# Kernel optimization log

Hardware: AMD Instinct MI355X
Metric: run time of the kernel (lower is better)

The kernel has to match this reference:

```python
import jax, jax.numpy as jnp
import numpy as np

BUCKET_SIZE = 128
HEADS = 8
HEAD_DIM = 64
LOOK_BACKWARD = 1
LOOK_FORWARD = 0  # causal => no look forward
TOKEN_SELF_ATTN_VALUE = -50000.0


def look_around(x, backward, forward, pad_value):
    n = x.shape[1]
    pw = [(0, 0)] * x.ndim
    pw[1] = (backward, forward)
    px = jnp.pad(x, pw, constant_values=pad_value)
    return jnp.concatenate([px[:, i:i + n] for i in range(backward + forward + 1)], axis=2)


def shift(x):
    # relative-shift trick: (..., i, j) -> (..., i, j)
    *lead, i, j = x.shape
    x = jnp.concatenate([x, jnp.zeros((*lead, i, i), x.dtype)], axis=-1)
    l = i + j - 1
    x = x.reshape(*lead, i * (i + j))
    pad = (-x.shape[-1]) % l
    x = jnp.concatenate([x, jnp.zeros((*lead, pad), x.dtype)], axis=-1)
    x = x.reshape(*lead, -1, l)
    return x[..., :i, i - 1:]


def setup_inputs() -> dict:
    key = jax.random.key(0)
    kq, kk, kv, kr = jax.random.split(key, 4)
    B, H, T, E = 2, HEADS, 8192, HEAD_DIM
    q = jax.random.normal(kq, (B, H, T, E), dtype=jnp.float32)
    k = jax.random.normal(kk, (B, H, T, E), dtype=jnp.float32)
    v = jax.random.normal(kv, (B, H, T, E), dtype=jnp.float32)
    rel_weights = jax.random.normal(kr, (2 * BUCKET_SIZE, H, E), dtype=jnp.float32)
    return {"q": q, "k": k, "v": v, "rel_weights": rel_weights}


def reference(q, k, v, rel_weights):
    B, H, T, E = q.shape
    qm = q.reshape(B * H, T, E)
    km = k.reshape(B * H, T, E)
    vm = v.reshape(B * H, T, E)

    # shared_qk: l2-normalize keys (F.normalize with eps=1e-12)
    km = km / jnp.maximum(jnp.linalg.norm(km, axis=-1, keepdims=True), 1e-12)

    buckets = T // BUCKET_SIZE
    bq = qm.reshape(B * H, buckets, BUCKET_SIZE, E)
    bk = km.reshape(B * H, buckets, BUCKET_SIZE, E)
    bv = vm.reshape(B * H, buckets, BUCKET_SIZE, E)

    bk = look_around(bk, LOOK_BACKWARD, LOOK_FORWARD, -1.0)
    bv = look_around(bv, LOOK_BACKWARD, LOOK_FORWARD, -1.0)

    ticker = jnp.arange(T, dtype=q.dtype)
    bq_t = ticker.reshape(1, buckets, BUCKET_SIZE)
    bq_k = look_around(bq_t, LOOK_BACKWARD, LOOK_FORWARD, -1.0)

    scale = E ** -0.5
    dots = jnp.einsum('bnie,bnje->bnij', bq, bk) * scale

    # relative positional bias
    bq5 = bq.reshape(B, H, buckets, BUCKET_SIZE, E)
    emb = jnp.einsum('bhnid,jhd->bhnij', bq5, rel_weights) * scale
    dots = dots + shift(emb).reshape(dots.shape)

    mask_value = -jnp.finfo(dots.dtype).max
    # shared_qk: mask self-attention positions
    self_mask = bq_t[:, :, :, None] == bq_k[:, :, None, :]
    dots = jnp.where(self_mask, TOKEN_SELF_ATTN_VALUE, dots)
    # causal mask
    causal_mask = bq_t[:, :, :, None] < bq_k[:, :, None, :]
    dots = jnp.where(causal_mask, mask_value, dots)
    # look-around padding mask
    pad_mask = (bq_k == -1.0)[:, :, None, :]
    dots = jnp.where(pad_mask, mask_value, dots)

    attn = jax.nn.softmax(dots, axis=-1)
    out = jnp.einsum('bnij,bnje->bnie', attn, bv)
    return out.reshape(B, H, T, E)
```

## Files before the change

### kernel.cpp

```cpp
#include <hip/hip_runtime.h>
#include <hip/hip_bf16.h>
#include <float.h>

#define NHEAD 8

typedef __attribute__((ext_vector_type(8))) short bf16x8;
typedef __attribute__((ext_vector_type(4))) float f32x4;

static __device__ __forceinline__ unsigned short bfb(float f) {
    __hip_bfloat16 h = __float2bfloat16(f);
    unsigned short u; __builtin_memcpy(&u, &h, 2); return u;
}
static __device__ __forceinline__ unsigned int pk2(float a, float b) {
    return (unsigned int)bfb(a) | ((unsigned int)bfb(b) << 16);
}
static __device__ __forceinline__ float bf2f_lo(unsigned int u) { return __uint_as_float(u << 16); }
static __device__ __forceinline__ float bf2f_hi(unsigned int u) { return __uint_as_float(u & 0xffff0000u); }

static __device__ __forceinline__ int swz64(int r, int c) {
    return (r << 6) + (c ^ ((r & 7) << 3));
}
static __device__ __forceinline__ int vIdx(int c, int kk) {
    return (c << 8) + (kk ^ ((c & 31) << 3));
}
static __device__ __forceinline__ int pIdx(int wv, int row, int col) {
    const int ch = (col >> 3) ^ (row & 3);
    return (wv * 16 + row) * 40 + ch * 8 + (col & 7);
}

static __device__ __forceinline__ f32x4 mfma16(bf16x8 a, bf16x8 b, f32x4 c) {
    return __builtin_amdgcn_mfma_f32_16x16x32_bf16(a, b, c, 0, 0, 0);
}

__global__ __launch_bounds__(512, 4)
void local_attn_kernel(const float* __restrict__ qg, const float* __restrict__ kg,
                       const float* __restrict__ vg, const float* __restrict__ rwg,
                       float* __restrict__ outg)
{
    __shared__ __align__(16) unsigned short sB[256 * 64];
    __shared__ __align__(16) unsigned short sRW[256 * 64];
    __shared__ __align__(16) unsigned short sP[8 * 16 * 40];

    const int tid  = threadIdx.x;
    const int lane = tid & 63;
    const int wv   = tid >> 6;
    const int jl   = lane & 15;
    const int hi   = lane >> 4;

    const int lb = ((blockIdx.x & 7) << 7) + (blockIdx.x >> 3);
    const int bh = lb >> 6;
    const int n  = lb & 63;
    const int h  = bh & 7;

    const float scale = 0.125f;
    const size_t bhOff = (size_t)bh * 8192 * 64;

    const float* Qp = qg + bhOff + (size_t)n * 128 * 64;
    const float* Kp = kg + bhOff + ((long)n - 1) * 128 * 64;
    const float* Vp = vg + bhOff + ((long)n - 1) * 128 * 64;

    const int cr = tid >> 4;
    const int c0 = (tid & 15) << 2;

    const int vc  = tid & 63;
    const int vkb = (tid >> 6) << 5;
    const bool vzero = (n == 0 && vkb < 128);
    unsigned int vpk[16];
    #pragma unroll
    for (int u = 0; u < 16; ++u) {
        float a = 0.f, b = 0.f;
        if (!vzero) {
            a = Vp[(vkb + 2 * u) * 64 + vc];
            b = Vp[(vkb + 2 * u + 1) * 64 + vc];
        }
        vpk[u] = pk2(a, b);
    }
    #pragma unroll
    for (int u = 0; u < 16; ++u)
        asm volatile("" :: "v"(vpk[u]));

    #pragma unroll
    for (int pp = 0; pp < 8; ++pp) {
        const int row = pp * 32 + cr;
        f32x4 x = {0.f, 0.f, 0.f, 0.f};
        if (!(n == 0 && row < 128))
            x = *reinterpret_cast<const f32x4*>(Kp + row * 64 + c0);
        float ss = x[0] * x[0] + x[1] * x[1] + x[2] * x[2] + x[3] * x[3];
        ss += __shfl_xor(ss, 1);
        ss += __shfl_xor(ss, 2);
        ss += __shfl_xor(ss, 4);
        ss += __shfl_xor(ss, 8);
        const float rn = 1.0f / fmaxf(sqrtf(ss), 1e-12f);
        ushort4 pkk = make_ushort4(bfb(x[0] * rn), bfb(x[1] * rn),
                                   bfb(x[2] * rn), bfb(x[3] * rn));
        *reinterpret_cast<ushort4*>(&sB[swz64(row, c0)]) = pkk;
    }

    #pragma unroll
    for (int pp = 0; pp < 8; ++pp) {
        const int row = pp * 32 + cr;
        const f32x4 x = *reinterpret_cast<const f32x4*>(rwg + ((size_t)row * NHEAD + h) * 64 + c0);
        ushort4 pkw = make_ushort4(bfb(x[0]), bfb(x[1]), bfb(x[2]), bfb(x[3]));
        *reinterpret_cast<ushort4*>(&sRW[swz64(row, c0)]) = pkw;
    }

    const int arow = wv * 16 + jl;
    const int kq0  = hi << 3;
    const float* qr = Qp + arow * 64 + kq0;
    const f32x4 qa = *reinterpret_cast<const f32x4*>(qr);
    const f32x4 qb = *reinterpret_cast<const f32x4*>(qr + 4);
    const f32x4 qc = *reinterpret_cast<const f32x4*>(qr + 32);
    const f32x4 qd = *reinterpret_cast<const f32x4*>(qr + 36);
    bf16x8 aq0, aq1;
    #pragma unroll
    for (int q = 0; q < 4; ++q) {
        aq0[q]     = (short)bfb(qa[q] * scale);
        aq0[q + 4] = (short)bfb(qb[q] * scale);
        aq1[q]     = (short)bfb(qc[q] * scale);
        aq1[q + 4] = (short)bfb(qd[q] * scale);
    }

    __syncthreads();

    const int tMax = wv + 8;

    f32x4 dots[16] = {};
    __builtin_amdgcn_s_setprio(1);
    #pragma unroll
    for (int t = 0; t < 16; ++t) {
        if (t <= tMax) {
            const int rr = t * 16 + jl;
            const bf16x8 b0 = *reinterpret_cast<const bf16x8*>(&sB[swz64(rr, kq0)]);
            const bf16x8 b1 = *reinterpret_cast<const bf16x8*>(&sB[swz64(rr, 32 + kq0)]);
            f32x4 d = {0.f, 0.f, 0.f, 0.f};
            d = mfma16(aq0, b0, d);
            d = mfma16(aq1, b1, d);
            dots[t] = d;
        }
    }
    __builtin_amdgcn_s_setprio(0);

    const int cv0 = 4 * hi + 1, cv1 = 4 * hi + 2, cv2 = 4 * hi + 3, cv3 = 4 * hi + 4;
    const int sl0 = (hi << 4) | ((jl - cv0) & 15);
    const int sl1 = (hi << 4) | ((jl - cv1) & 15);
    const int sl2 = (hi << 4) | ((jl - cv2) & 15);
    const int sl3 = (hi << 4) | ((jl - cv3) & 15);
    const bool g0 = jl >= cv0, g1 = jl >= cv1, g2 = jl >= cv2, g3 = jl >= cv3;

    unsigned int cur01, cur23;
    {
        const int rr = (7 - wv) * 16 + jl;
        const bf16x8 b0 = *reinterpret_cast<const bf16x8*>(&sRW[swz64(rr, kq0)]);
        const bf16x8 b1 = *reinterpret_cast<const bf16x8*>(&sRW[swz64(rr, 32 + kq0)]);
        f32x4 e = {0.f, 0.f, 0.f, 0.f};
        e = mfma16(aq0, b0, e);
        e = mfma16(aq1, b1, e);
        cur01 = pk2(e[0], e[1]);
        cur23 = pk2(e[2], e[3]);
    }
    unsigned int lo0 = (unsigned int)__shfl((int)cur01, sl0);
    unsigned int lo1 = (unsigned int)__shfl((int)cur01, sl1);
    unsigned int lo2 = (unsigned int)__shfl((int)cur23, sl2);
    unsigned int lo3 = (unsigned int)__shfl((int)cur23, sl3);

    unsigned int p01[16] = {}, p23[16] = {};
    float sm[4] = {0.f, 0.f, 0.f, 0.f};
    const bool npad = (n == 0);

    #pragma unroll
    for (int t = 0; t < 16; ++t) {
        if (t <= tMax) {
            unsigned int n01 = 0, n23 = 0;
            const int ts = t + 8 - wv;
            if (ts < 16) {
                const int rr2 = ts * 16 + jl;
                const bf16x8 e0 = *reinterpret_cast<const bf16x8*>(&sRW[swz64(rr2, kq0)]);
                const bf16x8 e1 = *reinterpret_cast<const bf16x8*>(&sRW[swz64(rr2, 32 + kq0)]);
                f32x4 e = {0.f, 0.f, 0.f, 0.f};
                e = mfma16(aq0, e0, e);
                e = mfma16(aq1, e1, e);
                n01 = pk2(e[0], e[1]);
                n23 = pk2(e[2], e[3]);
            }
            const unsigned int h0 = (unsigned int)__shfl((int)n01, sl0);
            const unsigned int h1 = (unsigned int)__shfl((int)n01, sl1);
            const unsigned int h2 = (unsigned int)__shfl((int)n23, sl2);
            const unsigned int h3 = (unsigned int)__shfl((int)n23, sl3);
            f32x4 d = dots[t];
            d[0] += bf2f_lo(g0 ? h0 : lo0);
            d[1] += bf2f_hi(g1 ? h1 : lo1);
            d[2] += bf2f_lo(g2 ? h2 : lo2);
            d[3] += bf2f_hi(g3 ? h3 : lo3);
            lo0 = h0; lo1 = h1; lo2 = h2; lo3 = h3;
            if (t >= 8 && t == tMax) {
                #pragma unroll
                for (int r = 0; r < 4; ++r) {
                    const int dd = 128 + jl - 4 * hi - r;
                    float x = d[r];
                    x = (dd == 128) ? -50.0f : x;
                    x = (dd > 128) ? -3.0e38f : x;
                    d[r] = x;
                }
            }
            if (t < 8 && npad) {
                #pragma unroll
                for (int r = 0; r < 4; ++r) d[r] = -3.0e38f;
            }
            f32x4 pe;
            #pragma unroll
            for (int r = 0; r < 4; ++r) {
                pe[r] = __expf(d[r]);
                sm[r] += pe[r];
            }
            p01[t] = pk2(pe[0], pe[1]);
            p23[t] = pk2(pe[2], pe[3]);
        }
    }

    float rinv[4];
    #pragma unroll
    for (int r = 0; r < 4; ++r) {
        sm[r] += __shfl_xor(sm[r], 1);
        sm[r] += __shfl_xor(sm[r], 2);
        sm[r] += __shfl_xor(sm[r], 4);
        sm[r] += __shfl_xor(sm[r], 8);
        rinv[r] = 1.0f / sm[r];
    }

    __syncthreads();

    #pragma unroll
    for (int w4 = 0; w4 < 4; ++w4) {
        const uint4 w = make_uint4(vpk[4 * w4], vpk[4 * w4 + 1],
                                   vpk[4 * w4 + 2], vpk[4 * w4 + 3]);
        *reinterpret_cast<uint4*>(&sB[vIdx(vc, vkb + 8 * w4)]) = w;
    }

    __syncthreads();

    f32x4 o[4] = {};
    #pragma unroll
    for (int pv = 0; pv < 8; ++pv) {
        if (2 * pv <= tMax) {
            #pragma unroll
            for (int tt = 0; tt < 2; ++tt) {
                const int t = 2 * pv + tt;
                const unsigned int w01 = p01[t];
                const unsigned int w23 = p23[t];
                const int col = tt * 16 + jl;
                sP[pIdx(wv, 4 * hi + 0, col)] = (unsigned short)w01;
                sP[pIdx(wv, 4 * hi + 1, col)] = (unsigned short)(w01 >> 16);
                sP[pIdx(wv, 4 * hi + 2, col)] = (unsigned short)w23;
                sP[pIdx(wv, 4 * hi + 3, col)] = (unsigned short)(w23 >> 16);
            }
            const bf16x8 pa = *reinterpret_cast<const bf16x8*>(&sP[pIdx(wv, jl, kq0)]);
            __builtin_amdgcn_s_setprio(1);
            #pragma unroll
            for (int ct = 0; ct < 4; ++ct) {
                const bf16x8 vb = *reinterpret_cast<const bf16x8*>(&sB[vIdx(ct * 16 + jl, pv * 32 + kq0)]);
                o[ct] = mfma16(pa, vb, o[ct]);
            }
            __builtin_amdgcn_s_setprio(0);
        }
    }

    const int ibase = wv * 16 + (hi << 2);
    float* Op = outg + bhOff + (size_t)n * 128 * 64;
    #pragma unroll
    for (int ct = 0; ct < 4; ++ct)
        #pragma unroll
        for (int r = 0; r < 4; ++r)
            Op[(ibase + r) * 64 + ct * 16 + jl] = o[ct][r] * rinv[r];
}

extern "C" void kernel_launch(void* const* d_in, const int* in_sizes, int n_in,
                              void* d_out, int out_size, void* d_ws, size_t ws_size,
                              hipStream_t stream) {
    const float* q  = (const float*)d_in[0];
    const float* k  = (const float*)d_in[1];
    const float* v  = (const float*)d_in[2];
    const float* rw = (const float*)d_in[3];
    float* out = (float*)d_out;
    local_attn_kernel<<<dim3(1024), dim3(512), 0, stream>>>(q, k, v, rw, out);
}
```

Before: 58.77 us.

## Process two buckets per 1024-thread block to share K/V/rel-weight loads

Each block now handles two adjacent query buckets with 16 waves, loading a 384-row K/V window and the relative-weight table once for both, so the overlapping neighbour bucket and the rel weights are no longer loaded and converted twice. V goes into its own LDS buffer with a new swizzle, which removes the extra barriers and the register staging of V. Softmax probabilities stay in the fp32 dots registers and are packed to bf16 only just before the PV step. The cost is a larger LDS footprint (about 128 KB) and launch bounds of 1024 threads with one block, which lowers occupancy and raises register pressure per wave.

```diff
diff --git a/kernel.cpp b/kernel.cpp
--- a/kernel.cpp
+++ b/kernel.cpp
@@ -21,7 +21,9 @@
     return (r << 6) + (c ^ ((r & 7) << 3));
 }
 static __device__ __forceinline__ int vIdx(int c, int kk) {
-    return (c << 8) + (kk ^ ((c & 31) << 3));
+    const int blk = kk >> 7, k7 = kk & 127;
+    const int ch  = ((k7 >> 3) ^ (c & 15));
+    return c * 384 + blk * 128 + ch * 8 + (kk & 7);
 }
 static __device__ __forceinline__ int pIdx(int wv, int row, int col) {
     const int ch = (col >> 3) ^ (row & 3);
@@ -32,59 +34,64 @@
     return __builtin_amdgcn_mfma_f32_16x16x32_bf16(a, b, c, 0, 0, 0);
 }
 
-__global__ __launch_bounds__(512, 4)
+__global__ __launch_bounds__(1024, 1)
 void local_attn_kernel(const float* __restrict__ qg, const float* __restrict__ kg,
                        const float* __restrict__ vg, const float* __restrict__ rwg,
                        float* __restrict__ outg)
 {
-    __shared__ __align__(16) unsigned short sB[256 * 64];
+    __shared__ __align__(16) unsigned short sK[384 * 64];
+    __shared__ __align__(16) unsigned short sV[64 * 384];
     __shared__ __align__(16) unsigned short sRW[256 * 64];
-    __shared__ __align__(16) unsigned short sP[8 * 16 * 40];
+    __shared__ __align__(16) unsigned short sP[16 * 16 * 40];
 
     const int tid  = threadIdx.x;
     const int lane = tid & 63;
     const int wv   = tid >> 6;
+    const int wvL  = wv & 7;
+    const int bkt  = wv >> 3;
     const int jl   = lane & 15;
     const int hi   = lane >> 4;
 
-    const int lb = ((blockIdx.x & 7) << 7) + (blockIdx.x >> 3);
-    const int bh = lb >> 6;
-    const int n  = lb & 63;
+    const int lb = ((blockIdx.x & 7) << 6) + (blockIdx.x >> 3);
+    const int bh = lb >> 5;
+    const int nb = (lb & 31) << 1;
     const int h  = bh & 7;
 
     const float scale = 0.125f;
     const size_t bhOff = (size_t)bh * 8192 * 64;
-
-    const float* Qp = qg + bhOff + (size_t)n * 128 * 64;
-    const float* Kp = kg + bhOff + ((long)n - 1) * 128 * 64;
-    const float* Vp = vg + bhOff + ((long)n - 1) * 128 * 64;
-
-    const int cr = tid >> 4;
-    const int c0 = (tid & 15) << 2;
-
-    const int vc  = tid & 63;
-    const int vkb = (tid >> 6) << 5;
-    const bool vzero = (n == 0 && vkb < 128);
-    unsigned int vpk[16];
-    #pragma unroll
-    for (int u = 0; u < 16; ++u) {
-        float a = 0.f, b = 0.f;
-        if (!vzero) {
-            a = Vp[(vkb + 2 * u) * 64 + vc];
-            b = Vp[(vkb + 2 * u + 1) * 64 + vc];
-        }
-        vpk[u] = pk2(a, b);
-    }
-    #pragma unroll
-    for (int u = 0; u < 16; ++u)
-        asm volatile("" :: "v"(vpk[u]));
-
-    #pragma unroll
-    for (int pp = 0; pp < 8; ++pp) {
-        const int row = pp * 32 + cr;
+    const int n = nb + bkt;
+
+    const float* Kw = kg + bhOff + ((long)nb - 1) * 128 * 64;
+    const float* Vw = vg + bhOff + ((long)nb - 1) * 128 * 64;
+
+    const int cr6 = tid >> 4;
+    const int c0  = (tid & 15) << 2;
+
+    {
+        const int vc = tid & 63;
+        const int vg0 = (tid >> 6) * 24;
+        unsigned int vp[12];
+        #pragma unroll
+        for (int u = 0; u < 12; ++u) {
+            const int k0 = vg0 + 2 * u;
+            float a = 0.f, b = 0.f;
+            if (!(nb == 0 && k0 < 128))       a = Vw[(size_t)k0 * 64 + vc];
+            if (!(nb == 0 && (k0 + 1) < 128)) b = Vw[(size_t)(k0 + 1) * 64 + vc];
+            vp[u] = pk2(a, b);
+        }
+        #pragma unroll
+        for (int w4 = 0; w4 < 3; ++w4) {
+            const uint4 w = make_uint4(vp[4 * w4], vp[4 * w4 + 1], vp[4 * w4 + 2], vp[4 * w4 + 3]);
+            *reinterpret_cast<uint4*>(&sV[vIdx(vc, vg0 + 8 * w4)]) = w;
+        }
+    }
+
+    #pragma unroll
+    for (int pp = 0; pp < 6; ++pp) {
+        const int row = pp * 64 + cr6;
         f32x4 x = {0.f, 0.f, 0.f, 0.f};
-        if (!(n == 0 && row < 128))
-            x = *reinterpret_cast<const f32x4*>(Kp + row * 64 + c0);
+        if (!(nb == 0 && row < 128))
+            x = *reinterpret_cast<const f32x4*>(Kw + (size_t)row * 64 + c0);
         float ss = x[0] * x[0] + x[1] * x[1] + x[2] * x[2] + x[3] * x[3];
         ss += __shfl_xor(ss, 1);
         ss += __shfl_xor(ss, 2);
@@ -93,20 +100,20 @@
         const float rn = 1.0f / fmaxf(sqrtf(ss), 1e-12f);
         ushort4 pkk = make_ushort4(bfb(x[0] * rn), bfb(x[1] * rn),
                                    bfb(x[2] * rn), bfb(x[3] * rn));
-        *reinterpret_cast<ushort4*>(&sB[swz64(row, c0)]) = pkk;
-    }
-
-    #pragma unroll
-    for (int pp = 0; pp < 8; ++pp) {
-        const int row = pp * 32 + cr;
+        *reinterpret_cast<ushort4*>(&sK[swz64(row, c0)]) = pkk;
+    }
+
+    #pragma unroll
+    for (int pp = 0; pp < 4; ++pp) {
+        const int row = pp * 64 + cr6;
         const f32x4 x = *reinterpret_cast<const f32x4*>(rwg + ((size_t)row * NHEAD + h) * 64 + c0);
         ushort4 pkw = make_ushort4(bfb(x[0]), bfb(x[1]), bfb(x[2]), bfb(x[3]));
         *reinterpret_cast<ushort4*>(&sRW[swz64(row, c0)]) = pkw;
     }
 
-    const int arow = wv * 16 + jl;
+    const int arow = wvL * 16 + jl;
     const int kq0  = hi << 3;
-    const float* qr = Qp + arow * 64 + kq0;
+    const float* qr = qg + bhOff + (size_t)n * 128 * 64 + arow * 64 + kq0;
     const f32x4 qa = *reinterpret_cast<const f32x4*>(qr);
     const f32x4 qb = *reinterpret_cast<const f32x4*>(qr + 4);
     const f32x4 qc = *reinterpret_cast<const f32x4*>(qr + 32);
@@ -122,16 +129,17 @@
 
     __syncthreads();
 
-    const int tMax = wv + 8;
+    const int tMax = wvL + 8;
+    const int bOff = bkt << 7;
 
     f32x4 dots[16] = {};
     __builtin_amdgcn_s_setprio(1);
     #pragma unroll
     for (int t = 0; t < 16; ++t) {
         if (t <= tMax) {
-            const int rr = t * 16 + jl;
-            const bf16x8 b0 = *reinterpret_cast<const bf16x8*>(&sB[swz64(rr, kq0)]);
-            const bf16x8 b1 = *reinterpret_cast<const bf16x8*>(&sB[swz64(rr, 32 + kq0)]);
+            const int rr = bOff + t * 16 + jl;
+            const bf16x8 b0 = *reinterpret_cast<const bf16x8*>(&sK[swz64(rr, kq0)]);
+            const bf16x8 b1 = *reinterpret_cast<const bf16x8*>(&sK[swz64(rr, 32 + kq0)]);
             f32x4 d = {0.f, 0.f, 0.f, 0.f};
             d = mfma16(aq0, b0, d);
             d = mfma16(aq1, b1, d);
@@ -149,7 +157,7 @@
 
     unsigned int cur01, cur23;
     {
-        const int rr = (7 - wv) * 16 + jl;
+        const int rr = (7 - wvL) * 16 + jl;
         const bf16x8 b0 = *reinterpret_cast<const bf16x8*>(&sRW[swz64(rr, kq0)]);
         const bf16x8 b1 = *reinterpret_cast<const bf16x8*>(&sRW[swz64(rr, 32 + kq0)]);
         f32x4 e = {0.f, 0.f, 0.f, 0.f};
@@ -163,7 +171,6 @@
     unsigned int lo2 = (unsigned int)__shfl((int)cur23, sl2);
     unsigned int lo3 = (unsigned int)__shfl((int)cur23, sl3);
 
-    unsigned int p01[16] = {}, p23[16] = {};
     float sm[4] = {0.f, 0.f, 0.f, 0.f};
     const bool npad = (n == 0);
 
@@ -171,7 +178,7 @@
     for (int t = 0; t < 16; ++t) {
         if (t <= tMax) {
             unsigned int n01 = 0, n23 = 0;
-            const int ts = t + 8 - wv;
+            const int ts = t + 8 - wvL;
             if (ts < 16) {
                 const int rr2 = ts * 16 + jl;
                 const bf16x8 e0 = *reinterpret_cast<const bf16x8*>(&sRW[swz64(rr2, kq0)]);
@@ -206,14 +213,13 @@
                 #pragma unroll
                 for (int r = 0; r < 4; ++r) d[r] = -3.0e38f;
             }
-            f32x4 pe;
             #pragma unroll
             for (int r = 0; r < 4; ++r) {
-                pe[r] = __expf(d[r]);
-                sm[r] += pe[r];
-            }
-            p01[t] = pk2(pe[0], pe[1]);
-            p23[t] = pk2(pe[2], pe[3]);
+                const float pe = __expf(d[r]);
+                d[r] = pe;
+                sm[r] += pe;
+            }
+            dots[t] = d;
         }
     }
 
@@ -227,17 +233,6 @@
         rinv[r] = 1.0f / sm[r];
     }
 
-    __syncthreads();
-
-    #pragma unroll
-    for (int w4 = 0; w4 < 4; ++w4) {
-        const uint4 w = make_uint4(vpk[4 * w4], vpk[4 * w4 + 1],
-                                   vpk[4 * w4 + 2], vpk[4 * w4 + 3]);
-        *reinterpret_cast<uint4*>(&sB[vIdx(vc, vkb + 8 * w4)]) = w;
-    }
-
-    __syncthreads();
-
     f32x4 o[4] = {};
     #pragma unroll
     for (int pv = 0; pv < 8; ++pv) {
@@ -245,8 +240,11 @@
             #pragma unroll
             for (int tt = 0; tt < 2; ++tt) {
                 const int t = 2 * pv + tt;
-                const unsigned int w01 = p01[t];
-                const unsigned int w23 = p23[t];
+                unsigned int w01 = 0, w23 = 0;
+                if (t <= tMax) {
+                    w01 = pk2(dots[t][0], dots[t][1]);
+                    w23 = pk2(dots[t][2], dots[t][3]);
+                }
                 const int col = tt * 16 + jl;
                 sP[pIdx(wv, 4 * hi + 0, col)] = (unsigned short)w01;
                 sP[pIdx(wv, 4 * hi + 1, col)] = (unsigned short)(w01 >> 16);
@@ -257,14 +255,14 @@
             __builtin_amdgcn_s_setprio(1);
             #pragma unroll
             for (int ct = 0; ct < 4; ++ct) {
-                const bf16x8 vb = *reinterpret_cast<const bf16x8*>(&sB[vIdx(ct * 16 + jl, pv * 32 + kq0)]);
+                const bf16x8 vb = *reinterpret_cast<const bf16x8*>(&sV[vIdx(ct * 16 + jl, bOff + pv * 32 + kq0)]);
                 o[ct] = mfma16(pa, vb, o[ct]);
             }
             __builtin_amdgcn_s_setprio(0);
         }
     }
 
-    const int ibase = wv * 16 + (hi << 2);
+    const int ibase = wvL * 16 + (hi << 2);
     float* Op = outg + bhOff + (size_t)n * 128 * 64;
     #pragma unroll
     for (int ct = 0; ct < 4; ++ct)
@@ -281,5 +279,5 @@
     const float* v  = (const float*)d_in[2];
     const float* rw = (const float*)d_in[3];
     float* out = (float*)d_out;
-    local_attn_kernel<<<dim3(1024), dim3(512), 0, stream>>>(q, k, v, rw, out);
-}
+    local_attn_kernel<<<dim3(512), dim3(1024), 0, stream>>>(q, k, v, rw, out);
+}
```

Result: no change. 58.88 us (+0.2%).

## Fuse QK scores and softmax into PV loop, stage V directly to LDS

Applied to the files above, without the earlier changes.

V is now written straight into a dedicated LDS buffer instead of being held in 16 packed registers until after softmax. The relative-position products are computed first from a bf16 copy of the weights staged in the shared buffer, then normalized K replaces them in the same buffer. The QK^T MFMAs, bias add, masking and exp are then computed per tile inside the PV loop, so the full dots/probability register arrays are gone and the final row-sum reduction moves to the end. This is meant to cut register pressure and interleave softmax with PV MFMAs, at the cost of two extra barriers and keeping K in registers across the relative-position phase.

```diff
diff --git a/kernel.cpp b/kernel.cpp
--- a/kernel.cpp
+++ b/kernel.cpp
@@ -38,7 +38,7 @@
                        float* __restrict__ outg)
 {
     __shared__ __align__(16) unsigned short sB[256 * 64];
-    __shared__ __align__(16) unsigned short sRW[256 * 64];
+    __shared__ __align__(16) unsigned short sV[64 * 256];
     __shared__ __align__(16) unsigned short sP[8 * 16 * 40];
 
     const int tid  = threadIdx.x;
@@ -62,46 +62,53 @@
     const int cr = tid >> 4;
     const int c0 = (tid & 15) << 2;
 
-    const int vc  = tid & 63;
-    const int vkb = (tid >> 6) << 5;
-    const bool vzero = (n == 0 && vkb < 128);
-    unsigned int vpk[16];
-    #pragma unroll
-    for (int u = 0; u < 16; ++u) {
-        float a = 0.f, b = 0.f;
-        if (!vzero) {
-            a = Vp[(vkb + 2 * u) * 64 + vc];
-            b = Vp[(vkb + 2 * u + 1) * 64 + vc];
+    {
+        const int vc  = tid & 63;
+        const int vkb = (tid >> 6) << 5;
+        const bool vzero = (n == 0 && vkb < 128);
+        #pragma unroll
+        for (int w4 = 0; w4 < 4; ++w4) {
+            unsigned int vp[4];
+            #pragma unroll
+            for (int u = 0; u < 4; ++u) {
+                const int k0 = vkb + 8 * w4 + 2 * u;
+                float a = 0.f, b = 0.f;
+                if (!vzero) {
+                    a = Vp[(size_t)k0 * 64 + vc];
+                    b = Vp[(size_t)(k0 + 1) * 64 + vc];
+                }
+                vp[u] = pk2(a, b);
+            }
+            *reinterpret_cast<uint4*>(&sV[vIdx(vc, vkb + 8 * w4)]) =
+                make_uint4(vp[0], vp[1], vp[2], vp[3]);
         }
-        vpk[u] = pk2(a, b);
-    }
-    #pragma unroll
-    for (int u = 0; u < 16; ++u)
-        asm volatile("" :: "v"(vpk[u]));
-
+    }
+
+    uint2 kpk[8];
     #pragma unroll
     for (int pp = 0; pp < 8; ++pp) {
         const int row = pp * 32 + cr;
         f32x4 x = {0.f, 0.f, 0.f, 0.f};
         if (!(n == 0 && row < 128))
-            x = *reinterpret_cast<const f32x4*>(Kp + row * 64 + c0);
+            x = *reinterpret_cast<const f32x4*>(Kp + (size_t)row * 64 + c0);
         float ss = x[0] * x[0] + x[1] * x[1] + x[2] * x[2] + x[3] * x[3];
         ss += __shfl_xor(ss, 1);
         ss += __shfl_xor(ss, 2);
         ss += __shfl_xor(ss, 4);
         ss += __shfl_xor(ss, 8);
         const float rn = 1.0f / fmaxf(sqrtf(ss), 1e-12f);
-        ushort4 pkk = make_ushort4(bfb(x[0] * rn), bfb(x[1] * rn),
-                                   bfb(x[2] * rn), bfb(x[3] * rn));
-        *reinterpret_cast<ushort4*>(&sB[swz64(row, c0)]) = pkk;
-    }
+        kpk[pp] = make_uint2(pk2(x[0] * rn, x[1] * rn), pk2(x[2] * rn, x[3] * rn));
+    }
+    #pragma unroll
+    for (int pp = 0; pp < 8; ++pp)
+        asm volatile("" :: "v"(kpk[pp].x), "v"(kpk[pp].y));
 
     #pragma unroll
     for (int pp = 0; pp < 8; ++pp) {
         const int row = pp * 32 + cr;
         const f32x4 x = *reinterpret_cast<const f32x4*>(rwg + ((size_t)row * NHEAD + h) * 64 + c0);
         ushort4 pkw = make_ushort4(bfb(x[0]), bfb(x[1]), bfb(x[2]), bfb(x[3]));
-        *reinterpret_cast<ushort4*>(&sRW[swz64(row, c0)]) = pkw;
+        *reinterpret_cast<ushort4*>(&sB[swz64(row, c0)]) = pkw;
     }
 
     const int arow = wv * 16 + jl;
@@ -124,21 +131,35 @@
 
     const int tMax = wv + 8;
 
-    f32x4 dots[16] = {};
+    unsigned int e01[17], e23[17];
     __builtin_amdgcn_s_setprio(1);
     #pragma unroll
-    for (int t = 0; t < 16; ++t) {
-        if (t <= tMax) {
-            const int rr = t * 16 + jl;
+    for (int s = 0; s < 17; ++s) {
+        unsigned int p01 = 0, p23 = 0;
+        const int ts = s + 7 - wv;
+        if (ts >= 0 && ts < 16) {
+            const int rr = ts * 16 + jl;
             const bf16x8 b0 = *reinterpret_cast<const bf16x8*>(&sB[swz64(rr, kq0)]);
             const bf16x8 b1 = *reinterpret_cast<const bf16x8*>(&sB[swz64(rr, 32 + kq0)]);
-            f32x4 d = {0.f, 0.f, 0.f, 0.f};
-            d = mfma16(aq0, b0, d);
-            d = mfma16(aq1, b1, d);
-            dots[t] = d;
+            f32x4 e = {0.f, 0.f, 0.f, 0.f};
+            e = mfma16(aq0, b0, e);
+            e = mfma16(aq1, b1, e);
+            p01 = pk2(e[0], e[1]);
+            p23 = pk2(e[2], e[3]);
         }
+        e01[s] = p01; e23[s] = p23;
     }
     __builtin_amdgcn_s_setprio(0);
+
+    __syncthreads();
+
+    #pragma unroll
+    for (int pp = 0; pp < 8; ++pp) {
+        const int row = pp * 32 + cr;
+        *reinterpret_cast<uint2*>(&sB[swz64(row, c0)]) = kpk[pp];
+    }
+
+    __syncthreads();
 
     const int cv0 = 4 * hi + 1, cv1 = 4 * hi + 2, cv2 = 4 * hi + 3, cv3 = 4 * hi + 4;
     const int sl0 = (hi << 4) | ((jl - cv0) & 15);
@@ -147,106 +168,61 @@
     const int sl3 = (hi << 4) | ((jl - cv3) & 15);
     const bool g0 = jl >= cv0, g1 = jl >= cv1, g2 = jl >= cv2, g3 = jl >= cv3;
 
-    unsigned int cur01, cur23;
-    {
-        const int rr = (7 - wv) * 16 + jl;
-        const bf16x8 b0 = *reinterpret_cast<const bf16x8*>(&sRW[swz64(rr, kq0)]);
-        const bf16x8 b1 = *reinterpret_cast<const bf16x8*>(&sRW[swz64(rr, 32 + kq0)]);
-        f32x4 e = {0.f, 0.f, 0.f, 0.f};
-        e = mfma16(aq0, b0, e);
-        e = mfma16(aq1, b1, e);
-        cur01 = pk2(e[0], e[1]);
-        cur23 = pk2(e[2], e[3]);
-    }
-    unsigned int lo0 = (unsigned int)__shfl((int)cur01, sl0);
-    unsigned int lo1 = (unsigned int)__shfl((int)cur01, sl1);
-    unsigned int lo2 = (unsigned int)__shfl((int)cur23, sl2);
-    unsigned int lo3 = (unsigned int)__shfl((int)cur23, sl3);
-
-    unsigned int p01[16] = {}, p23[16] = {};
+    unsigned int lo0 = (unsigned int)__shfl((int)e01[0], sl0);
+    unsigned int lo1 = (unsigned int)__shfl((int)e01[0], sl1);
+    unsigned int lo2 = (unsigned int)__shfl((int)e23[0], sl2);
+    unsigned int lo3 = (unsigned int)__shfl((int)e23[0], sl3);
+
     float sm[4] = {0.f, 0.f, 0.f, 0.f};
     const bool npad = (n == 0);
-
-    #pragma unroll
-    for (int t = 0; t < 16; ++t) {
-        if (t <= tMax) {
-            unsigned int n01 = 0, n23 = 0;
-            const int ts = t + 8 - wv;
-            if (ts < 16) {
-                const int rr2 = ts * 16 + jl;
-                const bf16x8 e0 = *reinterpret_cast<const bf16x8*>(&sRW[swz64(rr2, kq0)]);
-                const bf16x8 e1 = *reinterpret_cast<const bf16x8*>(&sRW[swz64(rr2, 32 + kq0)]);
-                f32x4 e = {0.f, 0.f, 0.f, 0.f};
-                e = mfma16(aq0, e0, e);
-                e = mfma16(aq1, e1, e);
-                n01 = pk2(e[0], e[1]);
-                n23 = pk2(e[2], e[3]);
-            }
-            const unsigned int h0 = (unsigned int)__shfl((int)n01, sl0);
-            const unsigned int h1 = (unsigned int)__shfl((int)n01, sl1);
-            const unsigned int h2 = (unsigned int)__shfl((int)n23, sl2);
-            const unsigned int h3 = (unsigned int)__shfl((int)n23, sl3);
-            f32x4 d = dots[t];
-            d[0] += bf2f_lo(g0 ? h0 : lo0);
-            d[1] += bf2f_hi(g1 ? h1 : lo1);
-            d[2] += bf2f_lo(g2 ? h2 : lo2);
-            d[3] += bf2f_hi(g3 ? h3 : lo3);
-            lo0 = h0; lo1 = h1; lo2 = h2; lo3 = h3;
-            if (t >= 8 && t == tMax) {
-                #pragma unroll
-                for (int r = 0; r < 4; ++r) {
-                    const int dd = 128 + jl - 4 * hi - r;
-                    float x = d[r];
-                    x = (dd == 128) ? -50.0f : x;
-                    x = (dd > 128) ? -3.0e38f : x;
-                    d[r] = x;
-                }
-            }
-            if (t < 8 && npad) {
-                #pragma unroll
-                for (int r = 0; r < 4; ++r) d[r] = -3.0e38f;
-            }
-            f32x4 pe;
-            #pragma unroll
-            for (int r = 0; r < 4; ++r) {
-                pe[r] = __expf(d[r]);
-                sm[r] += pe[r];
-            }
-            p01[t] = pk2(pe[0], pe[1]);
-            p23[t] = pk2(pe[2], pe[3]);
-        }
-    }
-
-    float rinv[4];
-    #pragma unroll
-    for (int r = 0; r < 4; ++r) {
-        sm[r] += __shfl_xor(sm[r], 1);
-        sm[r] += __shfl_xor(sm[r], 2);
-        sm[r] += __shfl_xor(sm[r], 4);
-        sm[r] += __shfl_xor(sm[r], 8);
-        rinv[r] = 1.0f / sm[r];
-    }
-
-    __syncthreads();
-
-    #pragma unroll
-    for (int w4 = 0; w4 < 4; ++w4) {
-        const uint4 w = make_uint4(vpk[4 * w4], vpk[4 * w4 + 1],
-                                   vpk[4 * w4 + 2], vpk[4 * w4 + 3]);
-        *reinterpret_cast<uint4*>(&sB[vIdx(vc, vkb + 8 * w4)]) = w;
-    }
-
-    __syncthreads();
-
     f32x4 o[4] = {};
+
     #pragma unroll
     for (int pv = 0; pv < 8; ++pv) {
         if (2 * pv <= tMax) {
             #pragma unroll
             for (int tt = 0; tt < 2; ++tt) {
                 const int t = 2 * pv + tt;
-                const unsigned int w01 = p01[t];
-                const unsigned int w23 = p23[t];
+                unsigned int w01 = 0, w23 = 0;
+                if (t <= tMax) {
+                    const int rr = t * 16 + jl;
+                    const bf16x8 b0 = *reinterpret_cast<const bf16x8*>(&sB[swz64(rr, kq0)]);
+                    const bf16x8 b1 = *reinterpret_cast<const bf16x8*>(&sB[swz64(rr, 32 + kq0)]);
+                    f32x4 d = {0.f, 0.f, 0.f, 0.f};
+                    d = mfma16(aq0, b0, d);
+                    d = mfma16(aq1, b1, d);
+                    const unsigned int h0 = (unsigned int)__shfl((int)e01[t + 1], sl0);
+                    const unsigned int h1 = (unsigned int)__shfl((int)e01[t + 1], sl1);
+                    const unsigned int h2 = (unsigned int)__shfl((int)e23[t + 1], sl2);
+                    const unsigned int h3 = (unsigned int)__shfl((int)e23[t + 1], sl3);
+                    d[0] += bf2f_lo(g0 ? h0 : lo0);
+                    d[1] += bf2f_hi(g1 ? h1 : lo1);
+                    d[2] += bf2f_lo(g2 ? h2 : lo2);
+                    d[3] += bf2f_hi(g3 ? h3 : lo3);
+                    lo0 = h0; lo1 = h1; lo2 = h2; lo3 = h3;
+                    if (t >= 8 && t == tMax) {
+                        #pragma unroll
+                        for (int r = 0; r < 4; ++r) {
+                            const int dd = 128 + jl - 4 * hi - r;
+                            float x = d[r];
+                            x = (dd == 128) ? -50.0f : x;
+                            x = (dd > 128) ? -3.0e38f : x;
+                            d[r] = x;
+                        }
+                    }
+                    if (t < 8 && npad) {
+                        #pragma unroll
+                        for (int r = 0; r < 4; ++r) d[r] = -3.0e38f;
+                    }
+                    f32x4 pe;
+                    #pragma unroll
+                    for (int r = 0; r < 4; ++r) {
+                        pe[r] = __expf(d[r]);
+                        sm[r] += pe[r];
+                    }
+                    w01 = pk2(pe[0], pe[1]);
+                    w23 = pk2(pe[2], pe[3]);
+                }
                 const int col = tt * 16 + jl;
                 sP[pIdx(wv, 4 * hi + 0, col)] = (unsigned short)w01;
                 sP[pIdx(wv, 4 * hi + 1, col)] = (unsigned short)(w01 >> 16);
@@ -257,13 +233,22 @@
             __builtin_amdgcn_s_setprio(1);
             #pragma unroll
             for (int ct = 0; ct < 4; ++ct) {
-                const bf16x8 vb = *reinterpret_cast<const bf16x8*>(&sB[vIdx(ct * 16 + jl, pv * 32 + kq0)]);
+                const bf16x8 vb = *reinterpret_cast<const bf16x8*>(&sV[vIdx(ct * 16 + jl, pv * 32 + kq0)]);
                 o[ct] = mfma16(pa, vb, o[ct]);
             }
             __builtin_amdgcn_s_setprio(0);
         }
     }
 
+    float rinv[4];
+    #pragma unroll
+    for (int r = 0; r < 4; ++r) {
+        sm[r] += __shfl_xor(sm[r], 1);
+        sm[r] += __shfl_xor(sm[r], 2);
+        sm[r] += __shfl_xor(sm[r], 4);
+        sm[r] += __shfl_xor(sm[r], 8);
+        rinv[r] = 1.0f / sm[r];
+    }
     const int ibase = wv * 16 + (hi << 2);
     float* Op = outg + bhOff + (size_t)n * 128 * 64;
     #pragma unroll
```

Result: faster. 48.48 us (median of 3 runs) (-17.5%).
